# Kernel tuning notes

Hardware: AMD Instinct MI355X
Metric: run time of the kernel (lower is better)

The kernel has to match this reference:

```python
import jax, jax.numpy as jnp
import numpy as np

T_SZ, T_STEP, T_CUT = 9, 6, 2
B, N, C, FS = 4, 2048, 512, 1
GRID = 120


def setup_inputs() -> dict:
    key = jax.random.key(0)
    rng = np.random.default_rng(0)
    ys = np.empty((B, N), np.int64)
    xs = np.empty((B, N), np.int64)
    for b in range(B):
        cells = rng.permutation(GRID * GRID)[:N]  # unique cells -> deterministic scatter
        ys[b] = cells // GRID
        xs[b] = cells % GRID
    features = jax.random.uniform(key, (B, N, C, FS, FS), jnp.float32)
    return {"features": features, "ys": jnp.asarray(ys), "xs": jnp.asarray(xs)}


def reference(features, ys, xs):
    # Faithful eager translation of TiledFeaturesMap.forward with validation=True
    # (y_rnd = x_rnd = 0, no random flips/transposes).
    f_tiles_list, f_ns_list = [], []
    for b in range(features.shape[0]):
        r = ys[b] > -1
        yv = ys[b][r]
        xv = xs[b][r]
        fv = features[b][r]                         # [nv, C, FS, FS]
        y_min, y_max = int(yv.min()), int(yv.max())
        x_min, x_max = int(xv.min()), int(xv.max())
        H = y_max - y_min + 1 + T_SZ
        W = x_max - x_min + 1 + T_SZ
        x_map = jnp.zeros((H, W, C, FS, FS), features.dtype).at[yv - y_min, xv - x_min].set(fv)
        nH = (H - T_SZ) // T_STEP + 1
        nW = (W - T_SZ) // T_STEP + 1
        ih = (jnp.arange(nH) * T_STEP)[:, None] + jnp.arange(T_SZ)[None, :]  # [nH, T_SZ]
        iw = (jnp.arange(nW) * T_STEP)[:, None] + jnp.arange(T_SZ)[None, :]  # [nW, T_SZ]
        # gather windows: [nH, nW, T_SZ, T_SZ, C, FS, FS]
        tiles = x_map[ih[:, None, :, None], iw[None, :, None, :]]
        # match torch unfold layout [nH, nW, C, FS, FS, T_SZ, T_SZ]
        tiles = tiles.transpose(0, 1, 4, 5, 6, 2, 3)
        center = tiles[..., T_CUT:-T_CUT, T_CUT:-T_CUT]
        sums = center.reshape(nH, nW, -1).sum(-1)
        mask = sums > 0
        if not bool(mask.any()):
            sums = tiles.reshape(nH, nW, -1).sum(-1)
            mask = sums > 0
        sel = tiles[mask]                            # [nt, C, FS, FS, T_SZ, T_SZ]
        f_tiles_list.append(sel)
        f_ns_list += [b] * int(mask.sum())
    f_tiles = jnp.concatenate(f_tiles_list, axis=0)
    f_ns = jnp.asarray(np.array(f_ns_list, np.int64))
    # permute(0,1,4,2,5,3): [Nt,C,FS,FS,T,T] -> [Nt,C,T,FS,T,FS] -> [Nt,C,T*FS,T*FS]
    f_tiles = f_tiles.transpose(0, 1, 4, 2, 5, 3).reshape(f_tiles.shape[0], C, T_SZ * FS, T_SZ * FS)
    return (f_ns, f_tiles)
```

## Files before the change

### kernel.cpp

```cpp
#include <hip/hip_runtime.h>
#include <hip/hip_bf16.h>
#include <limits.h>

#define BB   4
#define NN   2048
#define CC   512
#define TSZ  9
#define TSTEP 6
#define TCUT 2
#define GRIDW 120
#define CMS  132
#define CMSZ (CMS * CMS)
#define TILE_ELEMS (CC * TSZ * TSZ)
#define OUT_PER_TILE (TILE_ELEMS + 1)

__global__ void init_kernel(int4* __restrict__ cellmap4, int* __restrict__ bbox) {
    int i = blockIdx.x * blockDim.x + threadIdx.x;
    if (i < 16) bbox[i] = (i & 1) ? INT_MIN : INT_MAX;
    if (i < BB * CMSZ / 4) cellmap4[i] = make_int4(-1, -1, -1, -1);
}

__global__ void scatter_kernel(const int* __restrict__ ys, const int* __restrict__ xs,
                               int* __restrict__ cellmap, int* __restrict__ bbox) {
    int i = blockIdx.x * blockDim.x + threadIdx.x;
    if (i >= BB * NN) return;
    int b = i >> 11;
    int y = ys[i], x = xs[i];
    int ymin = INT_MAX, ymax = INT_MIN, xmin = INT_MAX, xmax = INT_MIN;
    if (y > -1) {
        cellmap[b * CMSZ + y * CMS + x] = i - b * NN;
        ymin = ymax = y; xmin = xmax = x;
    }
    #pragma unroll
    for (int off = 32; off; off >>= 1) {
        ymin = min(ymin, __shfl_xor(ymin, off));
        ymax = max(ymax, __shfl_xor(ymax, off));
        xmin = min(xmin, __shfl_xor(xmin, off));
        xmax = max(xmax, __shfl_xor(xmax, off));
    }
    if ((threadIdx.x & 63) == 0 && ymin != INT_MAX) {
        atomicMin(&bbox[b * 4 + 0], ymin);
        atomicMax(&bbox[b * 4 + 1], ymax);
        atomicMin(&bbox[b * 4 + 2], xmin);
        atomicMax(&bbox[b * 4 + 3], xmax);
    }
}

__global__ __launch_bounds__(512) void select_kernel(
        const int* __restrict__ bbox, const int* __restrict__ cellmap,
        int* __restrict__ tileinfo, float* __restrict__ f_ns) {
    __shared__ int s_off;
    __shared__ int s_wave[8];
    const int tid = threadIdx.x;
    const int lane = tid & 63;
    const int wid = tid >> 6;
    if (tid == 0) s_off = 0;
    __syncthreads();

    for (int b = 0; b < BB; ++b) {
        int ymin = bbox[b * 4 + 0];
        int ymax = bbox[b * 4 + 1];
        int xmin = bbox[b * 4 + 2];
        int xmax = bbox[b * 4 + 3];
        int nH = (ymax - ymin + 1) / TSTEP + 1;
        int nW = (xmax - xmin + 1) / TSTEP + 1;
        int nT = nH * nW;

        for (int base = 0; base < nT; base += 512) {
            int t = base + tid;
            bool m = false;
            int gy0 = 0, gx0 = 0;
            if (t < nT) {
                int ti = t / nW, tj = t - ti * nW;
                gy0 = ymin + ti * TSTEP;
                gx0 = xmin + tj * TSTEP;
                const int* __restrict__ base_p =
                    cellmap + b * CMSZ + (gy0 + TCUT) * CMS + (gx0 + TCUT);
                int acc = -1;
                #pragma unroll
                for (int dy = 0; dy < 5; ++dy)
                    #pragma unroll
                    for (int dx = 0; dx < 5; ++dx)
                        acc = max(acc, base_p[dy * CMS + dx]);
                m = (acc >= 0);
            }
            unsigned long long bal = __ballot(m);
            int lpre = __popcll(bal & ((1ull << lane) - 1ull));
            if (lane == 0) s_wave[wid] = (int)__popcll(bal);
            __syncthreads();
            if (tid == 0) {
                int acc = s_off;
                for (int w = 0; w < 8; ++w) { int v = s_wave[w]; s_wave[w] = acc; acc += v; }
                s_off = acc;
            }
            __syncthreads();
            if (m) {
                int idx = s_wave[wid] + lpre;
                tileinfo[idx] = (b << 16) | (gy0 << 8) | gx0;
                f_ns[idx] = (float)b;
            }
            __syncthreads();
        }
    }
}

__global__ __launch_bounds__(256) void fill_kernel(
        const float* __restrict__ feats, const int* __restrict__ cellmap,
        const int* __restrict__ tileinfo, float* __restrict__ out_tiles) {
    __shared__ int s_list[81];
    __shared__ int s_wcnt[2];
    __shared__ int s_cnt;
    __shared__ __align__(16) float s_f[64 * 81];

    const int tid = threadIdx.x;
    const int lane = tid & 63;
    const int wid = tid >> 6;
    const int k = blockIdx.x;

    const int info = tileinfo[k];
    const int b = info >> 16;
    const int gy0 = (info >> 8) & 255;
    const int gx0 = info & 255;

    const float4 z = make_float4(0.f, 0.f, 0.f, 0.f);
    for (int f4 = tid; f4 < 1296; f4 += 256) ((float4*)s_f)[f4] = z;

    int n = -1;
    if (tid < 81) {
        int r = tid / 9, c = tid - r * 9;
        n = cellmap[b * CMSZ + (gy0 + r) * CMS + (gx0 + c)];
    }
    bool occ = (tid < 81) && (n >= 0);
    unsigned long long bal = __ballot(occ);
    int pre = __popcll(bal & ((1ull << lane) - 1ull));
    if (lane == 0 && wid < 2) s_wcnt[wid] = (int)__popcll(bal);
    __syncthreads();
    if (occ) {
        int idx = (wid == 1 ? s_wcnt[0] : 0) + pre;
        s_list[idx] = (n << 7) | tid;
    }
    if (tid == 0) s_cnt = s_wcnt[0] + s_wcnt[1];
    __syncthreads();

    const int nk = s_cnt;
    const float* __restrict__ fb = feats + (size_t)b * (NN * CC);
    float* __restrict__ outk = out_tiles + (size_t)k * TILE_ELEMS;

    for (int cb = 0; cb < CC; cb += 64) {
        for (int e = tid; e < nk * 16; e += 256) {
            int slot = e >> 4, q = e & 15;
            int pk = s_list[slot];
            int pn = pk >> 7, ce = pk & 127;
            float4 v = *(const float4*)(fb + pn * CC + cb + q * 4);
            s_f[(q * 4 + 0) * 81 + ce] = v.x;
            s_f[(q * 4 + 1) * 81 + ce] = v.y;
            s_f[(q * 4 + 2) * 81 + ce] = v.z;
            s_f[(q * 4 + 3) * 81 + ce] = v.w;
        }
        __syncthreads();
        float* __restrict__ outc = outk + cb * 81;
        for (int f4 = tid; f4 < 1296; f4 += 256) {
            float4 v = ((const float4*)s_f)[f4];
            *(float4*)(outc + f4 * 4) = v;
        }
        __syncthreads();
    }
}

extern "C" void kernel_launch(void* const* d_in, const int* in_sizes, int n_in,
                              void* d_out, int out_size, void* d_ws, size_t ws_size,
                              hipStream_t stream) {
    const float* feats = (const float*)d_in[0];
    const int* ys = (const int*)d_in[1];
    const int* xs = (const int*)d_in[2];
    float* out = (float*)d_out;

    char* ws = (char*)d_ws;
    int* cellmap = (int*)ws;
    int* bbox = (int*)(ws + BB * CMSZ * 4);
    int* tileinfo = (int*)(ws + BB * CMSZ * 4 + 256);

    const int K = out_size / OUT_PER_TILE;
    float* f_ns = out;
    float* out_tiles = out + K;

    {
        int n4 = BB * CMSZ / 4;
        init_kernel<<<(n4 + 255) / 256, 256, 0, stream>>>((int4*)cellmap, bbox);
    }
    {
        int npt = BB * NN;
        scatter_kernel<<<(npt + 255) / 256, 256, 0, stream>>>(ys, xs, cellmap, bbox);
    }
    select_kernel<<<1, 512, 0, stream>>>(bbox, cellmap, tileinfo, f_ns);
    fill_kernel<<<K, 256, 0, stream>>>(feats, cellmap, tileinfo, out_tiles);
}
```

Before: 73.95 us.

## Fuse setup into one block kernel and split fill across channel chunks

Merges the init, scatter and select kernels into a single 1024-thread block that clears the cell map, scatters points, reduces bounding boxes in shared memory and compacts tiles. This removes two launches and the global atomics. The fill kernel now launches eight blocks per tile, one per 64-channel chunk, instead of looping over chunks, which gives far more parallelism and memory-level concurrency. The trade-offs are a serial single-block setup and a select loop that assumes at most 1024 candidate tiles per batch, plus the cell-map lookup being repeated in each chunk block.

```diff
diff --git a/kernel.cpp b/kernel.cpp
--- a/kernel.cpp
+++ b/kernel.cpp
@@ -14,93 +14,101 @@
 #define TILE_ELEMS (CC * TSZ * TSZ)
 #define OUT_PER_TILE (TILE_ELEMS + 1)
 
-__global__ void init_kernel(int4* __restrict__ cellmap4, int* __restrict__ bbox) {
-    int i = blockIdx.x * blockDim.x + threadIdx.x;
-    if (i < 16) bbox[i] = (i & 1) ? INT_MIN : INT_MAX;
-    if (i < BB * CMSZ / 4) cellmap4[i] = make_int4(-1, -1, -1, -1);
-}
-
-__global__ void scatter_kernel(const int* __restrict__ ys, const int* __restrict__ xs,
-                               int* __restrict__ cellmap, int* __restrict__ bbox) {
-    int i = blockIdx.x * blockDim.x + threadIdx.x;
-    if (i >= BB * NN) return;
-    int b = i >> 11;
-    int y = ys[i], x = xs[i];
-    int ymin = INT_MAX, ymax = INT_MIN, xmin = INT_MAX, xmax = INT_MIN;
-    if (y > -1) {
-        cellmap[b * CMSZ + y * CMS + x] = i - b * NN;
-        ymin = ymax = y; xmin = xmax = x;
-    }
-    #pragma unroll
-    for (int off = 32; off; off >>= 1) {
-        ymin = min(ymin, __shfl_xor(ymin, off));
-        ymax = max(ymax, __shfl_xor(ymax, off));
-        xmin = min(xmin, __shfl_xor(xmin, off));
-        xmax = max(xmax, __shfl_xor(xmax, off));
-    }
-    if ((threadIdx.x & 63) == 0 && ymin != INT_MAX) {
-        atomicMin(&bbox[b * 4 + 0], ymin);
-        atomicMax(&bbox[b * 4 + 1], ymax);
-        atomicMin(&bbox[b * 4 + 2], xmin);
-        atomicMax(&bbox[b * 4 + 3], xmax);
-    }
-}
-
-__global__ __launch_bounds__(512) void select_kernel(
-        const int* __restrict__ bbox, const int* __restrict__ cellmap,
-        int* __restrict__ tileinfo, float* __restrict__ f_ns) {
+__global__ __launch_bounds__(1024) void setup_kernel(
+        const int* __restrict__ ys, const int* __restrict__ xs,
+        int* __restrict__ cellmap, int* __restrict__ tileinfo,
+        float* __restrict__ f_ns) {
     __shared__ int s_off;
-    __shared__ int s_wave[8];
+    __shared__ int s_wave[16];
+    __shared__ int s_red[16][4];
+    __shared__ int s_bbox[4];
     const int tid = threadIdx.x;
     const int lane = tid & 63;
     const int wid = tid >> 6;
     if (tid == 0) s_off = 0;
+
+    int4* __restrict__ cm4 = (int4*)cellmap;
+    for (int i = tid; i < BB * CMSZ / 4; i += 1024)
+        cm4[i] = make_int4(-1, -1, -1, -1);
+    __syncthreads();
+
+    for (int i = tid; i < BB * NN; i += 1024) {
+        int y = ys[i], x = xs[i];
+        if (y > -1) {
+            int b = i >> 11;
+            cellmap[b * CMSZ + y * CMS + x] = i - (b << 11);
+        }
+    }
     __syncthreads();
 
     for (int b = 0; b < BB; ++b) {
-        int ymin = bbox[b * 4 + 0];
-        int ymax = bbox[b * 4 + 1];
-        int xmin = bbox[b * 4 + 2];
-        int xmax = bbox[b * 4 + 3];
+        int ymin = INT_MAX, ymax = INT_MIN, xmin = INT_MAX, xmax = INT_MIN;
+        for (int j = tid; j < NN; j += 1024) {
+            int y = ys[b * NN + j], x = xs[b * NN + j];
+            if (y > -1) {
+                ymin = min(ymin, y); ymax = max(ymax, y);
+                xmin = min(xmin, x); xmax = max(xmax, x);
+            }
+        }
+        #pragma unroll
+        for (int off = 32; off; off >>= 1) {
+            ymin = min(ymin, __shfl_xor(ymin, off));
+            ymax = max(ymax, __shfl_xor(ymax, off));
+            xmin = min(xmin, __shfl_xor(xmin, off));
+            xmax = max(xmax, __shfl_xor(xmax, off));
+        }
+        if (lane == 0) {
+            s_red[wid][0] = ymin; s_red[wid][1] = ymax;
+            s_red[wid][2] = xmin; s_red[wid][3] = xmax;
+        }
+        __syncthreads();
+        if (tid == 0) {
+            int a = INT_MAX, bx = INT_MIN, c = INT_MAX, d = INT_MIN;
+            for (int w = 0; w < 16; ++w) {
+                a = min(a, s_red[w][0]); bx = max(bx, s_red[w][1]);
+                c = min(c, s_red[w][2]); d = max(d, s_red[w][3]);
+            }
+            s_bbox[0] = a; s_bbox[1] = bx; s_bbox[2] = c; s_bbox[3] = d;
+        }
+        __syncthreads();
+        ymin = s_bbox[0]; ymax = s_bbox[1]; xmin = s_bbox[2]; xmax = s_bbox[3];
+
         int nH = (ymax - ymin + 1) / TSTEP + 1;
         int nW = (xmax - xmin + 1) / TSTEP + 1;
         int nT = nH * nW;
 
-        for (int base = 0; base < nT; base += 512) {
-            int t = base + tid;
-            bool m = false;
-            int gy0 = 0, gx0 = 0;
-            if (t < nT) {
-                int ti = t / nW, tj = t - ti * nW;
-                gy0 = ymin + ti * TSTEP;
-                gx0 = xmin + tj * TSTEP;
-                const int* __restrict__ base_p =
-                    cellmap + b * CMSZ + (gy0 + TCUT) * CMS + (gx0 + TCUT);
-                int acc = -1;
+        bool m = false;
+        int gy0 = 0, gx0 = 0;
+        if (tid < nT) {
+            int ti = tid / nW, tj = tid - ti * nW;
+            gy0 = ymin + ti * TSTEP;
+            gx0 = xmin + tj * TSTEP;
+            const int* __restrict__ bp =
+                cellmap + b * CMSZ + (gy0 + TCUT) * CMS + (gx0 + TCUT);
+            int acc = -1;
+            #pragma unroll
+            for (int dy = 0; dy < 5; ++dy)
                 #pragma unroll
-                for (int dy = 0; dy < 5; ++dy)
-                    #pragma unroll
-                    for (int dx = 0; dx < 5; ++dx)
-                        acc = max(acc, base_p[dy * CMS + dx]);
-                m = (acc >= 0);
-            }
-            unsigned long long bal = __ballot(m);
-            int lpre = __popcll(bal & ((1ull << lane) - 1ull));
-            if (lane == 0) s_wave[wid] = (int)__popcll(bal);
-            __syncthreads();
-            if (tid == 0) {
-                int acc = s_off;
-                for (int w = 0; w < 8; ++w) { int v = s_wave[w]; s_wave[w] = acc; acc += v; }
-                s_off = acc;
-            }
-            __syncthreads();
-            if (m) {
-                int idx = s_wave[wid] + lpre;
-                tileinfo[idx] = (b << 16) | (gy0 << 8) | gx0;
-                f_ns[idx] = (float)b;
-            }
-            __syncthreads();
+                for (int dx = 0; dx < 5; ++dx)
+                    acc = max(acc, bp[dy * CMS + dx]);
+            m = (acc >= 0);
         }
+        unsigned long long bal = __ballot(m);
+        int lpre = __popcll(bal & ((1ull << lane) - 1ull));
+        if (lane == 0) s_wave[wid] = (int)__popcll(bal);
+        __syncthreads();
+        if (tid == 0) {
+            int acc = s_off;
+            for (int w = 0; w < 16; ++w) { int v = s_wave[w]; s_wave[w] = acc; acc += v; }
+            s_off = acc;
+        }
+        __syncthreads();
+        if (m) {
+            int idx = s_wave[wid] + lpre;
+            tileinfo[idx] = (b << 16) | (gy0 << 8) | gx0;
+            f_ns[idx] = (float)b;
+        }
+        __syncthreads();
     }
 }
 
@@ -115,7 +123,8 @@
     const int tid = threadIdx.x;
     const int lane = tid & 63;
     const int wid = tid >> 6;
-    const int k = blockIdx.x;
+    const int k  = blockIdx.x >> 3;
+    const int cb = (blockIdx.x & 7) << 6;
 
     const int info = tileinfo[k];
     const int b = info >> 16;
@@ -143,27 +152,24 @@
     __syncthreads();
 
     const int nk = s_cnt;
-    const float* __restrict__ fb = feats + (size_t)b * (NN * CC);
-    float* __restrict__ outk = out_tiles + (size_t)k * TILE_ELEMS;
+    const float* __restrict__ fb = feats + (size_t)b * (NN * CC) + cb;
 
-    for (int cb = 0; cb < CC; cb += 64) {
-        for (int e = tid; e < nk * 16; e += 256) {
-            int slot = e >> 4, q = e & 15;
-            int pk = s_list[slot];
-            int pn = pk >> 7, ce = pk & 127;
-            float4 v = *(const float4*)(fb + pn * CC + cb + q * 4);
-            s_f[(q * 4 + 0) * 81 + ce] = v.x;
-            s_f[(q * 4 + 1) * 81 + ce] = v.y;
-            s_f[(q * 4 + 2) * 81 + ce] = v.z;
-            s_f[(q * 4 + 3) * 81 + ce] = v.w;
-        }
-        __syncthreads();
-        float* __restrict__ outc = outk + cb * 81;
-        for (int f4 = tid; f4 < 1296; f4 += 256) {
-            float4 v = ((const float4*)s_f)[f4];
-            *(float4*)(outc + f4 * 4) = v;
-        }
-        __syncthreads();
+    for (int e = tid; e < nk * 16; e += 256) {
+        int slot = e >> 4, q = e & 15;
+        int pk = s_list[slot];
+        int pn = pk >> 7, ce = pk & 127;
+        float4 v = *(const float4*)(fb + pn * CC + q * 4);
+        s_f[(q * 4 + 0) * 81 + ce] = v.x;
+        s_f[(q * 4 + 1) * 81 + ce] = v.y;
+        s_f[(q * 4 + 2) * 81 + ce] = v.z;
+        s_f[(q * 4 + 3) * 81 + ce] = v.w;
+    }
+    __syncthreads();
+
+    float* __restrict__ outc = out_tiles + (size_t)k * TILE_ELEMS + (size_t)cb * 81;
+    for (int f4 = tid; f4 < 1296; f4 += 256) {
+        float4 v = ((const float4*)s_f)[f4];
+        *(float4*)(outc + f4 * 4) = v;
     }
 }
 
@@ -177,21 +183,12 @@
 
     char* ws = (char*)d_ws;
     int* cellmap = (int*)ws;
-    int* bbox = (int*)(ws + BB * CMSZ * 4);
     int* tileinfo = (int*)(ws + BB * CMSZ * 4 + 256);
 
     const int K = out_size / OUT_PER_TILE;
     float* f_ns = out;
     float* out_tiles = out + K;
 
-    {
-        int n4 = BB * CMSZ / 4;
-        init_kernel<<<(n4 + 255) / 256, 256, 0, stream>>>((int4*)cellmap, bbox);
-    }
-    {
-        int npt = BB * NN;
-        scatter_kernel<<<(npt + 255) / 256, 256, 0, stream>>>(ys, xs, cellmap, bbox);
-    }
-    select_kernel<<<1, 512, 0, stream>>>(bbox, cellmap, tileinfo, f_ns);
-    fill_kernel<<<K, 256, 0, stream>>>(feats, cellmap, tileinfo, out_tiles);
+    setup_kernel<<<1, 1024, 0, stream>>>(ys, xs, cellmap, tileinfo, f_ns);
+    fill_kernel<<<K * 8, 256, 0, stream>>>(feats, cellmap, tileinfo, out_tiles);
 }
```

Result: slower. 77.25 us (+4.5%).
